# Performance work log

Measured on AMD Instinct MI355X. Metric: run time of the kernel, lower is better.

The kernel has to match this reference:

```python
import jax, jax.numpy as jnp
import numpy as np

EPS = 1e-6
FRAME_SEQLEN = 1560          # hardcoded in source kv-cache path
LOCAL_ATTN_SIZE = 4
MAX_ATTN = LOCAL_ATTN_SIZE * FRAME_SEQLEN  # 6240
NUM_HEADS = 12


def _ln(x, w=None, b=None):
    mu = jnp.mean(x, axis=-1, keepdims=True)
    var = jnp.mean(jnp.square(x - mu), axis=-1, keepdims=True)
    y = (x - mu) * jax.lax.rsqrt(var + EPS)
    return y * w + b if w is not None else y


def _rms(x, w):
    return x * jax.lax.rsqrt(jnp.mean(jnp.square(x), axis=-1, keepdims=True) + EPS) * w


def _rope_tables(freqs_real, freqs_imag, nf, hh, ww, start_frame, c):
    # split freqs columns into temporal / height / width parts, as in causal_rope_apply
    s0 = c - 2 * (c // 3)
    s1 = c // 3
    def build(tab):
        f0 = tab[start_frame:start_frame + nf, :s0]       # [nf, s0]
        f1 = tab[:hh, s0:s0 + s1]                          # [hh, s1]
        f2 = tab[:ww, s0 + s1:]                            # [ww, s1]
        return jnp.concatenate([
            jnp.broadcast_to(f0[:, None, None, :], (nf, hh, ww, s0)),
            jnp.broadcast_to(f1[None, :, None, :], (nf, hh, ww, s1)),
            jnp.broadcast_to(f2[None, None, :, :], (nf, hh, ww, s1)),
        ], axis=-1).reshape(nf * hh * ww, 1, c)
    return build(freqs_real), build(freqs_imag)


def _causal_rope(x, cos, sin):
    # x: [B, L, n, d] with interleaved (real, imag) pairs; cos/sin: [1, L, 1, c]
    B, L, n, d = x.shape
    c = d // 2
    xr = x.reshape(B, L, n, c, 2)
    a, b = xr[..., 0], xr[..., 1]
    out = jnp.stack([a * cos - b * sin, a * sin + b * cos], axis=-1)
    return out.reshape(B, L, n, d)


def _sdpa(q, k, v):
    scale = q.shape[-1] ** -0.5
    s = jnp.einsum('bqhd,bkhd->bhqk', q, k) * scale
    a = jax.nn.softmax(s, axis=-1)
    return jnp.einsum('bhqk,bkhd->bqhd', a, v)


def _forward(hidden_states, encoder_hidden_states, temb, freqs_real, freqs_imag,
             k_cache, v_cache, scale_shift_table,
             Wq, bq, Wk, bk, Wv, bv, Wo, bo, norm_q_w, norm_k_w,
             saln_w, saln_b,
             cWq, cbq, cWk, cbk, cWv, cbv, cWo, cbo, c_norm_q_w, c_norm_k_w,
             W1, b1, W2, b2,
             current_start, grid_h, grid_w):
    B, L, D = hidden_states.shape
    nf = temb.shape[1]
    fs = L // nf                     # == FRAME_SEQLEN
    H = NUM_HEADS
    hd = D // H
    c = hd // 2
    x = hidden_states.astype(jnp.float32)

    # AdaLN modulation per frame
    e = scale_shift_table + temb                     # [B, nf, 6, D]
    shift, scale, gate = e[:, :, 0:1], e[:, :, 1:2], e[:, :, 2:3]
    c_shift, c_scale, c_gate = e[:, :, 3:4], e[:, :, 4:5], e[:, :, 5:6]

    nh = (_ln(x).reshape(B, nf, fs, D) * (1 + scale) + shift).reshape(B, L, D)

    # self-attn projections + rms_norm_across_heads qk norm
    q = _rms(nh @ Wq.T + bq, norm_q_w).reshape(B, L, H, hd)
    k = _rms(nh @ Wk.T + bk, norm_k_w).reshape(B, L, H, hd)
    v = (nh @ Wv.T + bv).reshape(B, L, H, hd)

    # causal RoPE with temporal offset current_start // 1560
    start_frame = current_start // FRAME_SEQLEN
    cos, sin = _rope_tables(freqs_real, freqs_imag, nf, grid_h, grid_w, start_frame, c)
    cos, sin = cos[None], sin[None]                  # [1, L, 1, c]
    rq = _causal_rope(q, cos, sin)
    rk = _causal_rope(k, cos, sin)

    # kv-cache update (no-eviction branch: num_new + local_end_prev == cache size)
    kc = jax.lax.stop_gradient(k_cache).at[:, current_start:current_start + L].set(rk)
    vc = jax.lax.stop_gradient(v_cache).at[:, current_start:current_start + L].set(v)
    local_end = current_start + L
    win_lo = max(0, local_end - MAX_ATTN)
    attn = _sdpa(rq, kc[:, win_lo:local_end], vc[:, win_lo:local_end]).reshape(B, L, D)
    attn = attn @ Wo.T + bo

    # gated residual + affine LN (self_attn_residual_norm)
    x = x + (attn.reshape(B, nf, fs, D) * gate).reshape(B, L, D)
    n2 = _ln(x, saln_w, saln_b)

    # T2V cross attention
    ctx = encoder_hidden_states.astype(jnp.float32)
    Lc = ctx.shape[1]
    cq = _rms(n2 @ cWq.T + cbq, c_norm_q_w).reshape(B, L, H, hd)
    ck = _rms(ctx @ cWk.T + cbk, c_norm_k_w).reshape(B, Lc, H, hd)
    cv = (ctx @ cWv.T + cbv).reshape(B, Lc, H, hd)
    ca = _sdpa(cq, ck, cv).reshape(B, L, D) @ cWo.T + cbo

    # residual + LN with c_scale/c_shift modulation (cross_attn_residual_norm)
    x = x + ca
    n3 = (_ln(x).reshape(B, nf, fs, D) * (1 + c_scale) + c_shift).reshape(B, L, D)

    # FFN (gelu tanh) + gated residual (MulAdd)
    ff = jax.nn.gelu(n3 @ W1.T + b1, approximate=True) @ W2.T + b2
    x = x + (ff.reshape(B, nf, fs, D) * c_gate).reshape(B, L, D)
    return x


def setup_inputs() -> dict:
    key = jax.random.key(0)
    D, FF, H = 1536, 8960, NUM_HEADS
    NF, FS = 2, FRAME_SEQLEN
    L = NF * FS
    CACHE = MAX_ATTN
    CTX = 512
    hd = D // H
    c = hd // 2
    ks = iter(jax.random.split(key, 40))
    def nrm(shape, s=1.0):
        return jax.random.normal(next(ks), shape, jnp.float32) * s

    def part(dim):
        inv = 1.0 / (10000.0 ** (np.arange(0, dim, 2, dtype=np.float64) / dim))
        f = np.outer(np.arange(1024, dtype=np.float64), inv)
        return np.cos(f), np.sin(f)
    c0, s0 = part(2 * (c - 2 * (c // 3)))
    c1, s1 = part(2 * (c // 3))
    c2, s2 = part(2 * (c // 3))
    freqs_real = jnp.asarray(np.concatenate([c0, c1, c2], axis=1), jnp.float32)  # [1024, 64]
    freqs_imag = jnp.asarray(np.concatenate([s0, s1, s2], axis=1), jnp.float32)

    return dict(
        hidden_states=nrm((1, L, D)),
        encoder_hidden_states=nrm((1, CTX, D)),
        temb=nrm((1, NF, 6, D), 0.5),
        freqs_real=freqs_real, freqs_imag=freqs_imag,
        k_cache=nrm((1, CACHE, H, hd), 0.5),
        v_cache=nrm((1, CACHE, H, hd), 0.5),
        scale_shift_table=nrm((1, 6, D), D ** -0.5),
        Wq=nrm((D, D), 0.02), bq=jnp.zeros((D,), jnp.float32),
        Wk=nrm((D, D), 0.02), bk=jnp.zeros((D,), jnp.float32),
        Wv=nrm((D, D), 0.02), bv=jnp.zeros((D,), jnp.float32),
        Wo=nrm((D, D), 0.02), bo=jnp.zeros((D,), jnp.float32),
        norm_q_w=jnp.ones((D,), jnp.float32), norm_k_w=jnp.ones((D,), jnp.float32),
        saln_w=jnp.ones((D,), jnp.float32), saln_b=jnp.zeros((D,), jnp.float32),
        cWq=nrm((D, D), 0.02), cbq=jnp.zeros((D,), jnp.float32),
        cWk=nrm((D, D), 0.02), cbk=jnp.zeros((D,), jnp.float32),
        cWv=nrm((D, D), 0.02), cbv=jnp.zeros((D,), jnp.float32),
        cWo=nrm((D, D), 0.02), cbo=jnp.zeros((D,), jnp.float32),
        c_norm_q_w=jnp.ones((D,), jnp.float32), c_norm_k_w=jnp.ones((D,), jnp.float32),
        W1=nrm((FF, D), 0.02), b1=jnp.zeros((FF,), jnp.float32),
        W2=nrm((D, FF), 0.02), b2=jnp.zeros((D,), jnp.float32),
        current_start=2 * FS, grid_h=30, grid_w=52,
    )


def reference(hidden_states, encoder_hidden_states, temb, freqs_real, freqs_imag,
              k_cache, v_cache, scale_shift_table,
              Wq, bq, Wk, bk, Wv, bv, Wo, bo, norm_q_w, norm_k_w,
              saln_w, saln_b,
              cWq, cbq, cWk, cbk, cWv, cbv, cWo, cbo, c_norm_q_w, c_norm_k_w,
              W1, b1, W2, b2,
              current_start, grid_h, grid_w):
    return _forward(hidden_states, encoder_hidden_states, temb, freqs_real, freqs_imag,
                    k_cache, v_cache, scale_shift_table,
                    Wq, bq, Wk, bk, Wv, bv, Wo, bo, norm_q_w, norm_k_w,
                    saln_w, saln_b,
                    cWq, cbq, cWk, cbk, cWv, cbv, cWo, cbo, c_norm_q_w, c_norm_k_w,
                    W1, b1, W2, b2,
                    current_start, grid_h, grid_w)
```

## Files before the change

### kernel.cpp

```cpp
#include <hip/hip_runtime.h>
#include <hip/hip_bf16.h>
#include <stdint.h>

typedef uint16_t u16;
typedef uint32_t u32;
typedef float    f32x4  __attribute__((ext_vector_type(4)));
typedef __bf16   bf16x8 __attribute__((ext_vector_type(8)));
typedef u16      u16x8  __attribute__((ext_vector_type(8)));
typedef u16      u16x4  __attribute__((ext_vector_type(4)));
typedef u32      u32x2  __attribute__((ext_vector_type(2)));
typedef float    f32x4v __attribute__((ext_vector_type(4)));


__device__ __forceinline__ u16 f2bf(float f) {
    u32 u = __builtin_bit_cast(u32, f);
    u32 r = u + 0x7fffu + ((u >> 16) & 1u);
    return (u16)(r >> 16);
}
__device__ __forceinline__ float bfbits2f(u32 ubits) {
    return __builtin_bit_cast(float, ubits << 16);
}
__device__ __forceinline__ u32 cvtpk(float a, float b) {
    u32 r;
    asm("v_cvt_pk_bf16_f32 %0, %1, %2" : "=v"(r) : "v"(a), "v"(b));
    return r;
}
__device__ __forceinline__ bf16x8 loadb8(const u16* p) {
    u16x8 u = *(const u16x8*)p;
    return __builtin_bit_cast(bf16x8, u);
}
__device__ __forceinline__ f32x4 mfma16(bf16x8 a, bf16x8 b, f32x4 c) {
    return __builtin_amdgcn_mfma_f32_16x16x32_bf16(a, b, c, 0, 0, 0);
}
__device__ __forceinline__ void gload16(const u16* gp, u16* lp) {
    __builtin_amdgcn_global_load_lds((const __attribute__((address_space(1))) void*)gp,
                                     (__attribute__((address_space(3))) void*)lp, 16, 0, 0);
}
__device__ __forceinline__ float blockSum(float v, volatile float* buf, int t) {
#pragma unroll
    for (int o = 1; o < 64; o <<= 1) v += __shfl_xor(v, o);
    if ((t & 63) == 0) buf[t >> 6] = v;
    __syncthreads();
    float r = buf[0] + buf[1] + buf[2] + buf[3];
    __syncthreads();
    return r;
}

struct ConvJob { const float* s; u16* d; int n4; };
struct ConvJobs { ConvJob j[12]; int cnt; };

__global__ void k_conv(ConvJobs js) {
    int tid = blockIdx.x * blockDim.x + threadIdx.x;
    int stride = gridDim.x * blockDim.x;
    for (int q = 0; q < js.cnt; q++) {
        const f32x4v* s = (const f32x4v*)js.j[q].s;
        u16x4* d = (u16x4*)js.j[q].d;
        int n4 = js.j[q].n4;
        for (int i = tid; i < n4; i += stride) {
            f32x4v v = s[i];
            u16x4 o;
            o[0] = f2bf(v[0]); o[1] = f2bf(v[1]); o[2] = f2bf(v[2]); o[3] = f2bf(v[3]);
            d[i] = o;
        }
    }
}

__global__ void k_mod(const float* __restrict__ sst, const float* __restrict__ temb, float* __restrict__ e) {
    int i = blockIdx.x * 256 + threadIdx.x;
    if (i < 18432) e[i] = sst[i % 9216] + temb[i];
}

__global__ void k_cachecvt(const float* __restrict__ kc, const float* __restrict__ vc,
                           u16* __restrict__ Ka, u16* __restrict__ Va) {
    int b = blockIdx.x;
    int hd = (b % 6) * 256 + threadIdx.x;
    int p0 = (b / 6) * 16;
    int h = hd >> 7, d = hd & 127;
    u16x8 lo, hi;
#pragma unroll
    for (int j = 0; j < 16; j++) {
        long src = (long)(p0 + j) * 1536 + hd;
        Ka[(long)h * 798720 + (long)(p0 + j) * 128 + d] = f2bf(kc[src]);
        u16 v = f2bf(vc[src]);
        if (j < 8) lo[j] = v; else hi[j - 8] = v;
    }
    u16* dst = &Va[(long)h * 798720 + (long)d * 6240 + p0];
    *(u16x8*)dst = lo;
    *(u16x8*)(dst + 8) = hi;
}

__global__ __launch_bounds__(256) void k_ln(const float* __restrict__ x, u16* __restrict__ out,
                                            const float* __restrict__ mulp, const float* __restrict__ addp,
                                            int perFrame, int plusOne) {
    __shared__ float buf[4];
    const int row = blockIdx.x, t = threadIdx.x;
    const float* xr = x + (long)row * 1536;
    float v[6];
    float s = 0.f;
#pragma unroll
    for (int k = 0; k < 6; k++) { v[k] = xr[t + k * 256]; s += v[k]; }
    s = blockSum(s, buf, t);
    float mu = s * (1.f / 1536.f);
    float q = 0.f;
#pragma unroll
    for (int k = 0; k < 6; k++) { float d = v[k] - mu; q += d * d; }
    q = blockSum(q, buf, t);
    float inv = rsqrtf(q * (1.f / 1536.f) + 1e-6f);
    const int fo = perFrame ? (row / 1560) * 9216 : 0;
    u16* orow = out + (long)row * 1536;
    float add1 = plusOne ? 1.f : 0.f;
#pragma unroll
    for (int k = 0; k < 6; k++) {
        int c = t + k * 256;
        float m = mulp[fo + c] + add1;
        float y = (v[k] - mu) * inv * m + addp[fo + c];
        orow[c] = f2bf(y);
    }
}

__global__ __launch_bounds__(256) void k_rmsrope(const u16* __restrict__ in, int ld, int colOff,
                                                 const float* __restrict__ bias,
                                                 const float* __restrict__ w,
                                                 u16* __restrict__ out, long headStride,
                                                 const float* __restrict__ fr, const float* __restrict__ fi,
                                                 int doRope) {
    __shared__ float buf[4];
    const int row = blockIdx.x, t = threadIdx.x;
    const u32* xr = (const u32*)(in + (long)row * ld + colOff);
    const float2* b2 = (const float2*)bias;
    float px[3], py[3];
    float ss = 0.f;
#pragma unroll
    for (int i = 0; i < 3; i++) {
        u32 u = xr[t * 3 + i];
        float2 bb = b2[t * 3 + i];
        px[i] = bfbits2f(u & 0xffffu) + bb.x;
        py[i] = bfbits2f(u >> 16) + bb.y;
        ss += px[i] * px[i] + py[i] * py[i];
    }
    ss = blockSum(ss, buf, t);
    float inv = rsqrtf(ss * (1.f / 1536.f) + 1e-6f);
    int frame = 0, gh = 0, gw = 0;
    if (doRope) { frame = row / 1560; int rem = row - frame * 1560; gh = rem / 52; gw = rem - gh * 52; }
    const float2* w2 = (const float2*)w;
#pragma unroll
    for (int i = 0; i < 3; i++) {
        int jg = t * 3 + i;
        int hh = jg >> 6, j = jg & 63;
        float2 ww = w2[jg];
        float a = px[i] * inv * ww.x, b = py[i] * inv * ww.y;
        float oa = a, ob = b;
        if (doRope) {
            int fidx = (j < 22) ? (2 + frame) : ((j < 43) ? gh : gw);
            float cs = fr[fidx * 64 + j], sn = fi[fidx * 64 + j];
            oa = a * cs - b * sn;
            ob = a * sn + b * cs;
        }
        u16* dst = out + (long)hh * headStride + (long)row * 128 + j * 2;
        dst[0] = f2bf(oa);
        dst[1] = f2bf(ob);
    }
}

__global__ void k_scatterT(const u16* __restrict__ in, int ld, int colOff,
                           const float* __restrict__ bias, u16* __restrict__ outT,
                           int vstride, int posOff) {
    int hd = blockIdx.x * 256 + threadIdx.x;
    int r0 = blockIdx.y * 16;
    int h = hd >> 7, d = hd & 127;
    float bi = bias[hd];
    u16x8 lo, hi;
#pragma unroll
    for (int j = 0; j < 16; j++) {
        u16 v = f2bf(bfbits2f(in[(long)(r0 + j) * ld + colOff + hd]) + bi);
        if (j < 8) lo[j] = v; else hi[j - 8] = v;
    }
    u16* dst = &outT[(long)h * 128 * vstride + (long)d * vstride + posOff + r0];
    *(u16x8*)dst = lo;
    *(u16x8*)(dst + 8) = hi;
}

struct GemmP {
    const u16* A; const u16* B; void* C;
    const float* bias; const float* gate; const float* resid;
    int M, N, K, ldA, ldB, ldC, kChunk;
};

template <int EPI, int BM>
__global__ __launch_bounds__(256) void k_gemm(GemmP g) {
    constexpr int WM = BM / 2;
    constexpr int TM = BM / 32;
    __shared__ alignas(16) u16 As[BM * 32];
    __shared__ alignas(16) u16 Bs[128 * 32];
    const int t = threadIdx.x;
    const int w = t >> 6, l = t & 63, lr = l & 15, lg = l >> 4;
    const int wm = w >> 1, wn = w & 1;
    const long m0 = (long)blockIdx.y * BM, n0 = (long)blockIdx.x * 128;
    f32x4 acc[TM][4];
#pragma unroll
    for (int a = 0; a < TM; a++)
#pragma unroll
        for (int b = 0; b < 4; b++) acc[a][b] = f32x4{0.f, 0.f, 0.f, 0.f};

    const int rowU = t >> 2, c8 = t & 3;
    long arow[2], brow[2];
#pragma unroll
    for (int i = 0; i < 2; i++) {
        long r = m0 + rowU + i * 64;
        if (r > (long)g.M - 1) r = g.M - 1;
        arow[i] = r;
        brow[i] = n0 + rowU + i * 64;
    }

    const int kBeg = blockIdx.z * g.kChunk;
    const int kEnd = min(g.K, kBeg + g.kChunk);
    for (int k0 = kBeg; k0 < kEnd; k0 += 32) {
        __syncthreads();
#pragma unroll
        for (int i = 0; i < BM / 64; i++)
            gload16(g.A + arow[i] * (long)g.ldA + k0 + c8 * 8, &As[(i * 256 + w * 64) * 8]);
#pragma unroll
        for (int i = 0; i < 2; i++)
            gload16(g.B + brow[i] * (long)g.ldB + k0 + c8 * 8, &Bs[(i * 256 + w * 64) * 8]);
        __syncthreads();
        bf16x8 am[TM], bn[4];
#pragma unroll
        for (int mi = 0; mi < TM; mi++) am[mi] = loadb8(&As[(wm * WM + mi * 16 + lr) * 32 + lg * 8]);
#pragma unroll
        for (int ni = 0; ni < 4; ni++) bn[ni] = loadb8(&Bs[(wn * 64 + ni * 16 + lr) * 32 + lg * 8]);
#pragma unroll
        for (int mi = 0; mi < TM; mi++)
#pragma unroll
            for (int ni = 0; ni < 4; ni++)
                acc[mi][ni] = mfma16(am[mi], bn[ni], acc[mi][ni]);
    }

#pragma unroll
    for (int mi = 0; mi < TM; mi++) {
#pragma unroll
        for (int ni = 0; ni < 4; ni++) {
            long col = n0 + wn * 64 + ni * 16 + lr;
            float bi = g.bias ? g.bias[col] : 0.f;
#pragma unroll
            for (int r = 0; r < 4; r++) {
                long row = m0 + wm * WM + mi * 16 + lg * 4 + r;
                if (row >= g.M) continue;
                float v = acc[mi][ni][r] + bi;
                if constexpr (EPI == 0) {
                    ((float*)g.C)[row * g.ldC + col] = v;
                } else if constexpr (EPI == 1) {
                    ((u16*)g.C)[row * g.ldC + col] = f2bf(v);
                } else if constexpr (EPI == 2) {
                    float x3 = v * v * v;
                    float gl = 0.5f * v * (1.f + tanhf(0.79788456080286536f * (v + 0.044715f * x3)));
                    ((u16*)g.C)[row * g.ldC + col] = f2bf(gl);
                } else if constexpr (EPI == 3) {
                    float gt = g.gate ? g.gate[(row / 1560) * 9216 + col] : 1.f;
                    ((float*)g.C)[row * g.ldC + col] = g.resid[row * g.ldC + col] + v * gt;
                } else {
                    ((float*)g.C)[(long)blockIdx.z * ((long)g.M * g.ldC) + row * g.ldC + col] = v;
                }
            }
        }
    }
}

__global__ void k_gcomb(const float* __restrict__ P, int S, long MN4,
                        const float* __restrict__ bias, const float* __restrict__ gate,
                        const float* __restrict__ resid, float* __restrict__ out) {
    long i = (long)blockIdx.x * 256 + threadIdx.x;
    if (i >= MN4) return;
    f32x4v a = ((const f32x4v*)P)[i];
    for (int s = 1; s < S; s++) {
        f32x4v b = ((const f32x4v*)P)[(long)s * MN4 + i];
        a[0] += b[0]; a[1] += b[1]; a[2] += b[2]; a[3] += b[3];
    }
    long e0 = i * 4;
    int col = (int)(e0 % 1536);
    int fo = (int)((e0 / 1536) / 1560) * 9216;
    f32x4v r = ((const f32x4v*)resid)[i];
#pragma unroll
    for (int j = 0; j < 4; j++)
        r[j] += (a[j] + bias[col + j]) * gate[fo + col + j];
    ((f32x4v*)out)[i] = r;
}

__global__ void k_sumbf(const float* __restrict__ P, int S, long N4, u16* __restrict__ out) {
    long i = (long)blockIdx.x * 256 + threadIdx.x;
    if (i >= N4) return;
    f32x4v a = ((const f32x4v*)P)[i];
#pragma unroll 3
    for (int s = 1; s < S; s++) {
        f32x4v b = ((const f32x4v*)P)[(long)s * N4 + i];
        a[0] += b[0]; a[1] += b[1]; a[2] += b[2]; a[3] += b[3];
    }
    u16x4 o;
    o[0] = f2bf(a[0]); o[1] = f2bf(a[1]); o[2] = f2bf(a[2]); o[3] = f2bf(a[3]);
    ((u16x4*)out)[i] = o;
}

__global__ __launch_bounds__(256) void k_flash(const u16* __restrict__ Qb, const u16* __restrict__ Kb,
                                               const u16* __restrict__ Vtg,
                                               u16* __restrict__ Opart, float2* __restrict__ ms,
                                               int kvLen, int qlen, int splitIters, int totIters) {
    __shared__ alignas(16) u16 Kt[32 * 136];
    __shared__ alignas(16) u16 Vt[128 * 40];
    __shared__ alignas(16) u16 Pt[4][32 * 40];
    const int t = threadIdx.x;
    const int w = t >> 6, l = t & 63, lr = l & 15, lg = l >> 4;
    const int head = blockIdx.y, z = blockIdx.z;
    const long q0 = (long)blockIdx.x * 128;
    const u16* Qh = Qb + (long)head * qlen * 128;
    const u16* Kh = Kb + (long)head * kvLen * 128;
    const u16* Vh = Vtg + (long)head * kvLen * 128;
    constexpr float SCL2 = 0.08838834764831845f * 1.44269504088896f;

    bf16x8 aq[2][4];
#pragma unroll
    for (int wq = 0; wq < 2; wq++)
#pragma unroll
        for (int c = 0; c < 4; c++) {
            long row = q0 + w * 32 + wq * 16 + lr;
            if (row > (long)qlen - 1) row = qlen - 1;
            aq[wq][c] = loadb8(Qh + row * 128 + c * 32 + lg * 8);
        }

    f32x4 o[2][8];
    float mrow[2] = {-1e30f, -1e30f}, srow[2] = {0.f, 0.f};
#pragma unroll
    for (int wq = 0; wq < 2; wq++)
#pragma unroll
        for (int db = 0; db < 8; db++) o[wq][db] = f32x4{0.f, 0.f, 0.f, 0.f};

    const int kr = t >> 4, c16 = (t & 15) * 8;
    const int vr = t >> 1, vh = (t & 1) * 16;

    const int it0 = z * splitIters;
    const int itN = min(totIters, it0 + splitIters);
    for (int kt = it0; kt < itN; kt++) {
        const long k0 = (long)kt * 32;
        __syncthreads();
        {
            u16x8 a0 = *(const u16x8*)(Kh + (k0 + kr) * 128 + c16);
            u16x8 a1 = *(const u16x8*)(Kh + (k0 + kr + 16) * 128 + c16);
            *(u16x8*)&Kt[kr * 136 + c16] = a0;
            *(u16x8*)&Kt[(kr + 16) * 136 + c16] = a1;
            u16x8 b0 = *(const u16x8*)(Vh + (long)vr * kvLen + k0 + vh);
            u16x8 b1 = *(const u16x8*)(Vh + (long)vr * kvLen + k0 + vh + 8);
            *(u16x8*)&Vt[vr * 40 + vh] = b0;
            *(u16x8*)&Vt[vr * 40 + vh + 8] = b1;
        }
        __syncthreads();

        f32x4 s[2][2];
#pragma unroll
        for (int kh = 0; kh < 2; kh++) {
            bf16x8 kf[4];
#pragma unroll
            for (int cb = 0; cb < 4; cb++)
                kf[cb] = loadb8(&Kt[(kh * 16 + lr) * 136 + cb * 32 + lg * 8]);
#pragma unroll
            for (int wq = 0; wq < 2; wq++) {
                f32x4 acc = f32x4{0.f, 0.f, 0.f, 0.f};
#pragma unroll
                for (int cb = 0; cb < 4; cb++) acc = mfma16(kf[cb], aq[wq][cb], acc);
                s[wq][kh] = acc;
            }
        }

#pragma unroll
        for (int wq = 0; wq < 2; wq++) {
            float pml = fmaxf(fmaxf(fmaxf(s[wq][0][0], s[wq][0][1]), fmaxf(s[wq][0][2], s[wq][0][3])),
                              fmaxf(fmaxf(s[wq][1][0], s[wq][1][1]), fmaxf(s[wq][1][2], s[wq][1][3])));
            if (__any(pml * SCL2 > mrow[wq] + 8.f)) {
                float pm = fmaxf(pml, __shfl_xor(pml, 16));
                pm = fmaxf(pm, __shfl_xor(pm, 32));
                float nm = fmaxf(mrow[wq], pm * SCL2);
                float fsc = exp2f(mrow[wq] - nm);
                mrow[wq] = nm;
                srow[wq] *= fsc;
#pragma unroll
                for (int db = 0; db < 8; db++) {
                    f32x4 t4 = o[wq][db];
                    t4[0] *= fsc; t4[1] *= fsc; t4[2] *= fsc; t4[3] *= fsc;
                    o[wq][db] = t4;
                }
            }
            float p[8];
#pragma unroll
            for (int kh = 0; kh < 2; kh++)
#pragma unroll
                for (int r = 0; r < 4; r++)
                    p[kh * 4 + r] = exp2f(fmaf(s[wq][kh][r], SCL2, -mrow[wq]));
            srow[wq] += ((p[0] + p[1]) + (p[2] + p[3])) + ((p[4] + p[5]) + (p[6] + p[7]));
            u32x2 wa, wb;
            wa[0] = cvtpk(p[0], p[1]); wa[1] = cvtpk(p[2], p[3]);
            wb[0] = cvtpk(p[4], p[5]); wb[1] = cvtpk(p[6], p[7]);
            u16* pp = &Pt[w][(wq * 16 + lr) * 40 + lg * 4];
            *(u32x2*)pp = wa;
            *(u32x2*)(pp + 16) = wb;
        }

        bf16x8 pb0 = loadb8(&Pt[w][lr * 40 + lg * 8]);
        bf16x8 pb1 = loadb8(&Pt[w][(16 + lr) * 40 + lg * 8]);
#pragma unroll
        for (int db = 0; db < 8; db++) {
            bf16x8 vf = loadb8(&Vt[(db * 16 + lr) * 40 + lg * 8]);
            o[0][db] = mfma16(vf, pb0, o[0][db]);
            o[1][db] = mfma16(vf, pb1, o[1][db]);
        }
    }

#pragma unroll
    for (int wq = 0; wq < 2; wq++) {
        srow[wq] += __shfl_xor(srow[wq], 16);
        srow[wq] += __shfl_xor(srow[wq], 32);
    }

    const long part = ((long)z * 12 + head) * qlen;
#pragma unroll
    for (int wq = 0; wq < 2; wq++) {
        long row = q0 + w * 32 + wq * 16 + lr;
        if (row < qlen) {
            if (lg == 0) {
                float2 v; v.x = mrow[wq]; v.y = srow[wq];
                ms[part + row] = v;
            }
#pragma unroll
            for (int db = 0; db < 8; db++) {
                u16x4 pk;
#pragma unroll
                for (int r = 0; r < 4; r++) pk[r] = f2bf(o[wq][db][r]);
                *(u16x4*)&Opart[(part + row) * 128 + db * 16 + lg * 4] = pk;
            }
        }
    }
}

__global__ __launch_bounds__(256) void k_combine(const u16* __restrict__ Opart, const float2* __restrict__ ms,
                                                 u16* __restrict__ Ob, int qlen, int S) {
    int idx = blockIdx.x * 4 + (threadIdx.x >> 6);
    int l = threadIdx.x & 63;
    int h = idx / qlen, q = idx - h * qlen;
    float2 mm[6];
    float M = -1e30f;
    for (int s = 0; s < S; s++) {
        mm[s] = ms[((long)s * 12 + h) * qlen + q];
        M = fmaxf(M, mm[s].x);
    }
    float den = 0.f, a0 = 0.f, a1 = 0.f;
    for (int s = 0; s < S; s++) {
        float wgt = exp2f(mm[s].x - M);
        den += wgt * mm[s].y;
        u32 two = *(const u32*)&Opart[(((long)s * 12 + h) * qlen + q) * 128 + l * 2];
        a0 += wgt * bfbits2f(two & 0xffffu);
        a1 += wgt * bfbits2f(two >> 16);
    }
    float inv = 1.f / den;
    u32 o = ((u32)f2bf(a1 * inv) << 16) | (u32)f2bf(a0 * inv);
    *(u32*)&Ob[(long)q * 1536 + h * 128 + l * 2] = o;
}

extern "C" void kernel_launch(void* const* d_in, const int* in_sizes, int n_in,
                              void* d_out, int out_size, void* d_ws, size_t ws_size,
                              hipStream_t stream) {
    const float* hs    = (const float*)d_in[0];
    const float* ctx   = (const float*)d_in[1];
    const float* temb  = (const float*)d_in[2];
    const float* fr    = (const float*)d_in[3];
    const float* fi    = (const float*)d_in[4];
    const float* kcache= (const float*)d_in[5];
    const float* vcache= (const float*)d_in[6];
    const float* sst   = (const float*)d_in[7];
    const float* Wq = (const float*)d_in[8],  *bq = (const float*)d_in[9];
    const float* Wk = (const float*)d_in[10], *bk = (const float*)d_in[11];
    const float* Wv = (const float*)d_in[12], *bv = (const float*)d_in[13];
    const float* Wo = (const float*)d_in[14], *bo = (const float*)d_in[15];
    const float* nqw = (const float*)d_in[16], *nkw = (const float*)d_in[17];
    const float* salnw = (const float*)d_in[18], *salnb = (const float*)d_in[19];
    const float* cWq = (const float*)d_in[20], *cbq = (const float*)d_in[21];
    const float* cWk = (const float*)d_in[22], *cbk = (const float*)d_in[23];
    const float* cWv = (const float*)d_in[24], *cbv = (const float*)d_in[25];
    const float* cWo = (const float*)d_in[26], *cbo = (const float*)d_in[27];
    const float* cnqw = (const float*)d_in[28], *cnkw = (const float*)d_in[29];
    const float* W1 = (const float*)d_in[30], *b1 = (const float*)d_in[31];
    const float* W2 = (const float*)d_in[32], *b2 = (const float*)d_in[33];
    float* out = (float*)d_out;

    char* base = (char*)d_ws;
    size_t off = 0;
    auto alloc = [&](size_t bytes) -> char* {
        char* p = base + off;
        off = (off + bytes + 255) & ~(size_t)255;
        return p;
    };
    float* e   = (float*)alloc(18432 * 4);
    u16* nbuf  = (u16*)alloc((size_t)3120 * 1536 * 2);
    u16* lin   = (u16*)alloc((size_t)3120 * 4608 * 2);
    u16* Qb    = (u16*)alloc((size_t)12 * 3120 * 128 * 2);
    u16* Ka    = (u16*)alloc((size_t)12 * 6240 * 128 * 2);
    u16* Va    = (u16*)alloc((size_t)12 * 6240 * 128 * 2);
    u16* attnb = (u16*)alloc((size_t)3120 * 1536 * 2);
    float* X1  = (float*)alloc((size_t)3120 * 1536 * 4);
    u16* CKb   = (u16*)alloc((size_t)12 * 512 * 128 * 2);
    u16* CVt   = (u16*)alloc((size_t)12 * 512 * 128 * 2);
    u16* H1    = (u16*)alloc((size_t)3120 * 8960 * 2);
    u16* wqkv_b= (u16*)alloc((size_t)4608 * 1536 * 2);
    u16* wo_b  = (u16*)alloc((size_t)1536 * 1536 * 2);
    u16* cwq_b = (u16*)alloc((size_t)1536 * 1536 * 2);
    u16* cwkv_b= (u16*)alloc((size_t)3072 * 1536 * 2);
    u16* cwo_b = (u16*)alloc((size_t)1536 * 1536 * 2);
    u16* w1_b  = (u16*)alloc((size_t)8960 * 1536 * 2);
    u16* w2_b  = (u16*)alloc((size_t)8960 * 1536 * 2);
    u16* ctxb  = (u16*)alloc((size_t)512 * 1536 * 2);

    u16* Opart = H1;
    float2* msb = (float2*)lin;
    float* pbuf = (float*)lin;
    float* cpart = (float*)H1;

    ConvJobs cj{};
    auto setj = [&](int i, const float* s, u16* d, int n) { cj.j[i].s = s; cj.j[i].d = d; cj.j[i].n4 = n / 4; };
    setj(0, Wq, wqkv_b, 1536 * 1536);
    setj(1, Wk, wqkv_b + (size_t)1536 * 1536, 1536 * 1536);
    setj(2, Wv, wqkv_b + (size_t)2 * 1536 * 1536, 1536 * 1536);
    setj(3, Wo, wo_b, 1536 * 1536);
    setj(4, cWq, cwq_b, 1536 * 1536);
    setj(5, cWk, cwkv_b, 1536 * 1536);
    setj(6, cWv, cwkv_b + (size_t)1536 * 1536, 1536 * 1536);
    setj(7, cWo, cwo_b, 1536 * 1536);
    setj(8, W1, w1_b, 8960 * 1536);
    setj(9, W2, w2_b, 8960 * 1536);
    setj(10, ctx, ctxb, 512 * 1536);
    cj.cnt = 11;
    k_conv<<<2048, 256, 0, stream>>>(cj);

    k_mod<<<72, 256, 0, stream>>>(sst, temb, e);
    k_cachecvt<<<1170, 256, 0, stream>>>(kcache, vcache, Ka, Va);

    k_ln<<<3120, 256, 0, stream>>>(hs, nbuf, e + 1536, e + 0, 1, 1);

    GemmP gqkv{nbuf, wqkv_b, lin, nullptr, nullptr, nullptr, 3120, 4608, 1536, 1536, 1536, 4608, 1536};
    k_gemm<1, 64><<<dim3(36, 49), 256, 0, stream>>>(gqkv);
    k_rmsrope<<<3120, 256, 0, stream>>>(lin, 4608, 0, bq, nqw, Qb, (long)3120 * 128, fr, fi, 1);
    k_rmsrope<<<3120, 256, 0, stream>>>(lin, 4608, 1536, bk, nkw, Ka + (size_t)3120 * 128, (long)6240 * 128, fr, fi, 1);
    k_scatterT<<<dim3(6, 195), 256, 0, stream>>>(lin, 4608, 3072, bv, Va, 6240, 3120);

    k_flash<<<dim3(25, 12, 5), 256, 0, stream>>>(Qb, Ka, Va, Opart, msb, 6240, 3120, 39, 195);
    k_combine<<<9360, 256, 0, stream>>>(Opart, msb, attnb, 3120, 5);

    GemmP gwo{attnb, wo_b, X1, bo, e + 2 * 1536, hs, 3120, 1536, 1536, 1536, 1536, 1536, 1536};
    k_gemm<3, 64><<<dim3(12, 49), 256, 0, stream>>>(gwo);

    k_ln<<<3120, 256, 0, stream>>>(X1, nbuf, salnw, salnb, 0, 0);

    GemmP gcq{nbuf, cwq_b, lin, nullptr, nullptr, nullptr, 3120, 1536, 1536, 1536, 1536, 1536, 1536};
    k_gemm<1, 64><<<dim3(12, 49), 256, 0, stream>>>(gcq);
    k_rmsrope<<<3120, 256, 0, stream>>>(lin, 1536, 0, cbq, cnqw, Qb, (long)3120 * 128, fr, fi, 0);

    GemmP gckv{ctxb, cwkv_b, cpart, nullptr, nullptr, nullptr, 512, 3072, 1536, 1536, 1536, 3072, 384};
    k_gemm<5, 64><<<dim3(24, 8, 4), 256, 0, stream>>>(gckv);
    k_sumbf<<<1536, 256, 0, stream>>>(cpart, 4, 393216, lin);
    k_rmsrope<<<512, 256, 0, stream>>>(lin, 3072, 0, cbk, cnkw, CKb, (long)512 * 128, fr, fi, 0);
    k_scatterT<<<dim3(6, 32), 256, 0, stream>>>(lin, 3072, 1536, cbv, CVt, 512, 0);

    k_flash<<<dim3(25, 12, 4), 256, 0, stream>>>(Qb, CKb, CVt, Opart, msb, 512, 3120, 4, 16);
    k_combine<<<9360, 256, 0, stream>>>(Opart, msb, attnb, 3120, 4);

    GemmP gcwo{attnb, cwo_b, X1, cbo, nullptr, X1, 3120, 1536, 1536, 1536, 1536, 1536, 1536};
    k_gemm<3, 64><<<dim3(12, 49), 256, 0, stream>>>(gcwo);

    k_ln<<<3120, 256, 0, stream>>>(X1, nbuf, e + 4 * 1536, e + 3 * 1536, 1, 1);

    GemmP g1{nbuf, w1_b, H1, b1, nullptr, nullptr, 3120, 8960, 1536, 1536, 1536, 8960, 1536};
    k_gemm<2, 128><<<dim3(70, 25), 256, 0, stream>>>(g1);

    GemmP g2{H1, w2_b, pbuf, nullptr, nullptr, nullptr, 3120, 1536, 8960, 8960, 8960, 1536, 4480};
    k_gemm<5, 64><<<dim3(12, 49, 2), 256, 0, stream>>>(g2);
    k_gcomb<<<4680, 256, 0, stream>>>(pbuf, 2, 1198080, b2, e + 5 * 1536, X1, out);
}
```

Before: 1.064 ms.

## Add 256x256-tile 512-thread GEMM kernel for QKV and FFN1 projections

Introduces a new GEMM kernel with 256x256 output tiles, 8 waves, double-buffered swizzled LDS and a phased MFMA schedule that interleaves the next tile's global loads with compute and raises wave priority around the MFMAs. It replaces the 64/128-wide tile kernels for the QKV projection and the first FFN GEMM, aiming to raise arithmetic intensity and cut global/LDS traffic per FLOP. The trade-off is 128 KB of LDS per block and heavy register use. Fewer blocks (234 and 455) may also underfill the CUs and leave wave quantization tails.

After: 1.051 ms. Within noise of the previous version (-1.2%).

```diff
diff --git a/kernel.cpp b/kernel.cpp
--- a/kernel.cpp
+++ b/kernel.cpp
@@ -259,6 +259,109 @@
                     ((float*)g.C)[row * g.ldC + col] = g.resid[row * g.ldC + col] + v * gt;
                 } else {
                     ((float*)g.C)[(long)blockIdx.z * ((long)g.M * g.ldC) + row * g.ldC + col] = v;
+                }
+            }
+        }
+    }
+}
+
+template <int EPI>
+__global__ __launch_bounds__(512, 2) void k_gemm256(GemmP g) {
+    __shared__ alignas(16) u16 As[2][16384];
+    __shared__ alignas(16) u16 Bs[2][16384];
+    const int t = threadIdx.x;
+    const int wid = t >> 6, l = t & 63, lr = l & 15, lg = l >> 4;
+    const int wm = wid >> 2, wn = wid & 3;
+    const long m0 = (long)blockIdx.y * 256, n0 = (long)blockIdx.x * 256;
+    const int nt = g.K >> 6;
+
+    f32x4 acc[8][4];
+#pragma unroll
+    for (int a = 0; a < 8; a++)
+#pragma unroll
+        for (int b = 0; b < 4; b++) acc[a][b] = f32x4{0.f, 0.f, 0.f, 0.f};
+
+    const int su = t >> 3;
+    const int sc = t & 7;
+    const int ldsBase = (wid << 9);
+
+    auto stA = [&](int b, int tk, int j) {
+        int r = j * 64 + su;
+        long row = m0 + r; if (row > (long)g.M - 1) row = g.M - 1;
+        gload16(g.A + row * (long)g.ldA + tk * 64 + ((sc ^ (r & 7)) * 8),
+                &As[b][(j << 12) + ldsBase]);
+    };
+    auto stB = [&](int b, int tk, int j) {
+        int r = j * 64 + su;
+        long row = n0 + r; if (row > (long)g.N - 1) row = g.N - 1;
+        gload16(g.B + row * (long)g.ldB + tk * 64 + ((sc ^ (r & 7)) * 8),
+                &Bs[b][(j << 12) + ldsBase]);
+    };
+
+#pragma unroll
+    for (int j = 0; j < 4; j++) stA(0, 0, j);
+#pragma unroll
+    for (int j = 0; j < 4; j++) stB(0, 0, j);
+    __syncthreads();
+
+    for (int tk = 0; tk < nt; ++tk) {
+        const int cur = tk & 1, nxt = cur ^ 1;
+        const bool pre = (tk + 1 < nt);
+        bf16x8 bB[4][2];
+#pragma unroll
+        for (int ph = 0; ph < 4; ++ph) {
+            if (pre) {
+                if (ph == 0) { stA(nxt, tk + 1, 0); stA(nxt, tk + 1, 1); stA(nxt, tk + 1, 2); stA(nxt, tk + 1, 3); }
+                else if (ph == 1) { stB(nxt, tk + 1, 0); stB(nxt, tk + 1, 1); stB(nxt, tk + 1, 2); stB(nxt, tk + 1, 3); }
+            }
+            if (ph == 0) {
+#pragma unroll
+                for (int ni = 0; ni < 4; ni++)
+#pragma unroll
+                    for (int kk = 0; kk < 2; kk++) {
+                        int row = wn * 64 + ni * 16 + lr;
+                        bB[ni][kk] = loadb8(&Bs[cur][row * 64 + (((kk * 4 + lg) ^ (lr & 7)) * 8)]);
+                    }
+            }
+            bf16x8 aA[2][2];
+#pragma unroll
+            for (int mi2 = 0; mi2 < 2; mi2++)
+#pragma unroll
+                for (int kk = 0; kk < 2; kk++) {
+                    int row = wm * 128 + (ph * 2 + mi2) * 16 + lr;
+                    aA[mi2][kk] = loadb8(&As[cur][row * 64 + (((kk * 4 + lg) ^ (lr & 7)) * 8)]);
+                }
+            __builtin_amdgcn_s_setprio(1);
+#pragma unroll
+            for (int mi2 = 0; mi2 < 2; mi2++)
+#pragma unroll
+                for (int ni = 0; ni < 4; ni++)
+#pragma unroll
+                    for (int kk = 0; kk < 2; kk++)
+                        acc[ph * 2 + mi2][ni] = mfma16(aA[mi2][kk], bB[ni][kk], acc[ph * 2 + mi2][ni]);
+            __builtin_amdgcn_s_setprio(0);
+            __builtin_amdgcn_sched_barrier(0);
+        }
+        __syncthreads();
+    }
+
+#pragma unroll
+    for (int mi = 0; mi < 8; mi++) {
+#pragma unroll
+        for (int ni = 0; ni < 4; ni++) {
+            long col = n0 + wn * 64 + ni * 16 + lr;
+            float bi = g.bias ? g.bias[col] : 0.f;
+#pragma unroll
+            for (int r = 0; r < 4; r++) {
+                long row = m0 + wm * 128 + mi * 16 + lg * 4 + r;
+                if (row >= g.M) continue;
+                float v = acc[mi][ni][r] + bi;
+                if constexpr (EPI == 1) {
+                    ((u16*)g.C)[row * g.ldC + col] = f2bf(v);
+                } else {
+                    float x3 = v * v * v;
+                    float gl = 0.5f * v * (1.f + tanhf(0.79788456080286536f * (v + 0.044715f * x3)));
+                    ((u16*)g.C)[row * g.ldC + col] = f2bf(gl);
                 }
             }
         }
@@ -541,7 +644,7 @@
     k_ln<<<3120, 256, 0, stream>>>(hs, nbuf, e + 1536, e + 0, 1, 1);
 
     GemmP gqkv{nbuf, wqkv_b, lin, nullptr, nullptr, nullptr, 3120, 4608, 1536, 1536, 1536, 4608, 1536};
-    k_gemm<1, 64><<<dim3(36, 49), 256, 0, stream>>>(gqkv);
+    k_gemm256<1><<<dim3(18, 13), 512, 0, stream>>>(gqkv);
     k_rmsrope<<<3120, 256, 0, stream>>>(lin, 4608, 0, bq, nqw, Qb, (long)3120 * 128, fr, fi, 1);
     k_rmsrope<<<3120, 256, 0, stream>>>(lin, 4608, 1536, bk, nkw, Ka + (size_t)3120 * 128, (long)6240 * 128, fr, fi, 1);
     k_scatterT<<<dim3(6, 195), 256, 0, stream>>>(lin, 4608, 3072, bv, Va, 6240, 3120);
@@ -573,7 +676,7 @@
     k_ln<<<3120, 256, 0, stream>>>(X1, nbuf, e + 4 * 1536, e + 3 * 1536, 1, 1);
 
     GemmP g1{nbuf, w1_b, H1, b1, nullptr, nullptr, 3120, 8960, 1536, 1536, 1536, 8960, 1536};
-    k_gemm<2, 128><<<dim3(70, 25), 256, 0, stream>>>(g1);
+    k_gemm256<2><<<dim3(35, 13), 512, 0, stream>>>(g1);
 
     GemmP g2{H1, w2_b, pbuf, nullptr, nullptr, nullptr, 3120, 1536, 8960, 8960, 8960, 1536, 4480};
     k_gemm<5, 64><<<dim3(12, 49, 2), 256, 0, stream>>>(g2);
```
